# Kernel tuning notes

Hardware: AMD Instinct MI355X
Metric: run time of the kernel (lower is better)

## Reference

```python
import jax, jax.numpy as jnp
import numpy as np

WS = 8          # window size
NUM_HEADS = 3
DIM = 96
HIDDEN = int(DIM * 2.0)
LN_EPS = 1e-5


def _rel_pos_index(ws):
    coords = np.stack(np.meshgrid(np.arange(ws), np.arange(ws), indexing='ij'))  # (2,ws,ws)
    cf = coords.reshape(2, -1)                          # (2, N)
    rel = cf[:, :, None] - cf[:, None, :]               # (2, N, N)
    rel = rel.transpose(1, 2, 0).astype(np.int64)       # (N, N, 2)
    rel[:, :, 0] += ws - 1
    rel[:, :, 1] += ws - 1
    rel[:, :, 0] *= 2 * ws - 1
    return jnp.asarray(rel.sum(-1))                     # (N, N)


def _layernorm(x, g, b):
    mu = jnp.mean(x, axis=-1, keepdims=True)
    var = jnp.mean(jnp.square(x - mu), axis=-1, keepdims=True)
    return (x - mu) * jax.lax.rsqrt(var + LN_EPS) * g + b


def setup_inputs() -> dict:
    key = jax.random.key(0)
    ks = jax.random.split(key, 10)
    C = DIM
    std = 0.02
    return {
        'x': jax.random.normal(ks[0], (8, C, 256, 256), dtype=jnp.float32),
        'qkv_w': jax.random.normal(ks[1], (3 * C, C), dtype=jnp.float32) * std,
        'qkv_b': jnp.zeros((3 * C,), dtype=jnp.float32),
        'proj_w': jax.random.normal(ks[2], (C, C), dtype=jnp.float32) * std,
        'proj_b': jnp.zeros((C,), dtype=jnp.float32),
        'rpb_table': jax.random.normal(ks[3], ((2 * WS - 1) ** 2, NUM_HEADS), dtype=jnp.float32) * std,
        'norm1_g': jnp.ones((C,), dtype=jnp.float32),
        'norm1_b': jnp.zeros((C,), dtype=jnp.float32),
        'norm2_g': jnp.ones((C,), dtype=jnp.float32),
        'norm2_b': jnp.zeros((C,), dtype=jnp.float32),
        'fc1_w': jax.random.normal(ks[4], (HIDDEN, C), dtype=jnp.float32) * std,
        'fc1_b': jnp.zeros((HIDDEN,), dtype=jnp.float32),
        'fc2_w': jax.random.normal(ks[5], (C, HIDDEN), dtype=jnp.float32) * std,
        'fc2_b': jnp.zeros((C,), dtype=jnp.float32),
        'H': 256,
        'W': 256,
    }


def reference(x, qkv_w, qkv_b, proj_w, proj_b, rpb_table,
              norm1_g, norm1_b, norm2_g, norm2_b,
              fc1_w, fc1_b, fc2_w, fc2_b, H, W):
    B, C, Hc, Wc = x.shape
    ws = WS
    nh, nw = H // ws, W // ws
    N = ws * ws
    heads = NUM_HEADS
    hd = C // heads

    # window partition: (B,C,H,W) -> (B*nh*nw, N, C)
    xp = jnp.transpose(x, (0, 2, 3, 1))
    xw = xp.reshape(B, nh, ws, nw, ws, C).transpose(0, 1, 3, 2, 4, 5)
    xw = xw.reshape(B * nh * nw, N, C)

    xw = _layernorm(xw, norm1_g, norm1_b)

    # window attention
    B_ = B * nh * nw
    qkv = xw @ qkv_w.T + qkv_b                                  # (B_, N, 3C)
    qkv = qkv.reshape(B_, N, 3, heads, hd).transpose(2, 0, 3, 1, 4)
    q, k, v = qkv[0], qkv[1], qkv[2]                            # (B_, h, N, d)
    q = q * (hd ** -0.5)
    attn = jnp.einsum('bhnd,bhmd->bhnm', q, k)                  # (B_, h, N, N)
    rpi = _rel_pos_index(ws)                                    # (N, N)
    bias = rpb_table[rpi.reshape(-1)].reshape(N, N, heads).transpose(2, 0, 1)
    attn = jax.nn.softmax(attn + bias[None], axis=-1)
    out = jnp.einsum('bhnm,bhmd->bhnd', attn, v)                # (B_, h, N, d)
    out = out.transpose(0, 2, 1, 3).reshape(B_, N, C)
    out = out @ proj_w.T + proj_b

    # norm2 + MLP (note: original applies them sequentially, single residual at end)
    out = _layernorm(out, norm2_g, norm2_b)
    h = jax.nn.gelu(out @ fc1_w.T + fc1_b, approximate=False)
    out = h @ fc2_w.T + fc2_b

    # window merge + residual
    out = out.reshape(B, nh, nw, ws, ws, C).transpose(0, 5, 1, 3, 2, 4)
    out = out.reshape(B, C, H, W)
    return out + x
```

## Files before the change

kernel.cpp:

```cpp
#include <hip/hip_runtime.h>
#include <hip/hip_bf16.h>

using bf16 = __hip_bfloat16;
typedef short short8  __attribute__((ext_vector_type(8)));
typedef short short4v __attribute__((ext_vector_type(4)));
typedef float f32x4   __attribute__((ext_vector_type(4)));

static __device__ __forceinline__ bf16  f2b(float v){ return __float2bfloat16(v); }
static __device__ __forceinline__ float s2f(short s){ return __bfloat162float(__builtin_bit_cast(bf16, s)); }
static __device__ __forceinline__ short f2s(float f){ return __builtin_bit_cast(short, __float2bfloat16(f)); }

static __device__ __forceinline__ short8 ldw8(const float* __restrict__ p){
  const float4 u = *(const float4*)(p);
  const float4 v = *(const float4*)(p + 4);
  short8 r;
  r[0]=f2s(u.x); r[1]=f2s(u.y); r[2]=f2s(u.z); r[3]=f2s(u.w);
  r[4]=f2s(v.x); r[5]=f2s(v.y); r[6]=f2s(v.z); r[7]=f2s(v.w);
  return r;
}

#define MFMA16(a,b,c) __builtin_amdgcn_mfma_f32_16x16x32_bf16((a),(b),(c),0,0,0)

#define KEYR(row) ((((row) >> 2) & 3) << 4)

constexpr int TPB = 256;
constexpr float EPS = 1e-5f;
constexpr float QSC = 0.17677669529663687f;

constexpr int WQ_OFF  = 0;
constexpr int WPJ_OFF = 27648;
constexpr int WF1_OFF = 36864;
constexpr int WF2_OFF = 55296;
constexpr int WTOT    = 73728;
constexpr int BTAB_BYTE_OFF = 147456;
constexpr size_t WS_NEEDED = 147456 + 49152;

constexpr int R0_OFF = 0;
constexpr int R1_OFF = 26624;
constexpr int R2_OFF = 53248;
constexpr int SMEM_BYTES = 80896;

__global__ void init_ws_kernel(
    const float* __restrict__ qkvw, const float* __restrict__ projw,
    const float* __restrict__ fc1w, const float* __restrict__ fc2w,
    const float* __restrict__ rpb,
    bf16* __restrict__ wbf, float* __restrict__ btab)
{
  const int i = blockIdx.x * 256 + threadIdx.x;
  if (i < WTOT){
    float v;
    if (i < WPJ_OFF)      v = qkvw[i];
    else if (i < WF1_OFF) v = projw[i - WPJ_OFF];
    else if (i < WF2_OFF) v = fc1w[i - WF1_OFF];
    else                  v = fc2w[i - WF2_OFF];
    if (i < 9216) v *= QSC;
    wbf[i] = f2b(v);
  }
  if (i < 3*64*64){
    const int h   = i >> 12;
    const int row = (i >> 6) & 63;
    const int col = i & 63;
    const int rel = ((row>>3) - (col>>3) + 7)*15 + ((row&7) - (col&7) + 7);
    btab[i] = rpb[rel*3 + h];
  }
}

template<bool PRE>
__global__ __launch_bounds__(TPB, 2) void swin_block_kernel(
    const float* __restrict__ x,
    const float* __restrict__ qkvw,  const float* __restrict__ qkvb,
    const float* __restrict__ projw, const float* __restrict__ projb,
    const float* __restrict__ rpb,
    const float* __restrict__ n1g,   const float* __restrict__ n1b,
    const float* __restrict__ n2g,   const float* __restrict__ n2b,
    const float* __restrict__ fc1w,  const float* __restrict__ fc1b,
    const float* __restrict__ fc2w,  const float* __restrict__ fc2b,
    float* __restrict__ out,
    const bf16* __restrict__ wbf,    const float* __restrict__ btab)
{
  __shared__ alignas(16) unsigned char smem[SMEM_BYTES];
  char* s_a  = (char*)(smem + R0_OFF);
  char* s_q  = (char*)(smem + R0_OFF);
  char* s_k  = (char*)(smem + R0_OFF + 10240);
  char* s_at = (char*)(smem + R0_OFF);
  char* s_ao = (char*)(smem + R1_OFF);
  char* s_h  = (char*)(smem + R1_OFF);
  char* s_vt = (char*)(smem + R2_OFF);
  char* s_p  = (char*)(smem + R2_OFF + 9216);

  const bf16* wQ  = wbf + WQ_OFF;
  const bf16* wP  = wbf + WPJ_OFF;
  const bf16* wF1 = wbf + WF1_OFF;
  const bf16* wF2 = wbf + WF2_OFF;

  const int tid  = threadIdx.x;
  const int wid  = tid >> 6;
  const int lane = tid & 63;
  const int quad = lane >> 4;
  const int l15  = lane & 15;
  const int m0   = wid * 16;
  const int row0 = m0 + quad * 4;
  const int cwz  = quad << 4;
  const int rwz  = ((l15 >> 2) & 3) << 4;

  const int blk = blockIdx.x;
  const int b    = blk >> 9;
  const int wh   = (blk >> 4) & 31;
  const int wcol = blk & 15;
  const size_t base = ((size_t)b * 96) * 65536 + (size_t)wh * 2048 + (size_t)wcol * 16;

  float4 xsave[12];
  #pragma unroll
  for (int it = 0; it < 12; it++){
    const int idx4 = it*256 + tid;
    const int c = idx4 >> 5, r = idx4 & 31;
    const int irow = r >> 2, j0 = (r & 3) * 4;
    const float4 xv = *(const float4*)(x + base + (size_t)c*65536 + irow*256 + j0);
    xsave[it] = xv;
    const int srow = (j0 >> 3)*64 + irow*8 + (j0 & 7);
    const int co = (c*2) ^ KEYR(srow);
    *(bf16*)(s_a + (srow+0)*208 + co) = f2b(xv.x);
    *(bf16*)(s_a + (srow+1)*208 + co) = f2b(xv.y);
    *(bf16*)(s_a + (srow+2)*208 + co) = f2b(xv.z);
    *(bf16*)(s_a + (srow+3)*208 + co) = f2b(xv.w);
  }
  __syncthreads();

  {
    const int rr = tid >> 2, s = tid & 3;
    const int cb = s*24;
    const int key = KEYR(rr);
    float gv[24], bb[24];
    #pragma unroll
    for (int u = 0; u < 6; u++){
      const float4 g4 = *(const float4*)(n1g + cb + u*4);
      const float4 b4 = *(const float4*)(n1b + cb + u*4);
      gv[u*4+0]=g4.x; gv[u*4+1]=g4.y; gv[u*4+2]=g4.z; gv[u*4+3]=g4.w;
      bb[u*4+0]=b4.x; bb[u*4+1]=b4.y; bb[u*4+2]=b4.z; bb[u*4+3]=b4.w;
    }
    #pragma unroll
    for (int wv = 0; wv < 2; wv++){
      char* row = s_a + (wv*64 + rr)*208;
      float vals[24];
      float sum = 0.f, sq = 0.f;
      #pragma unroll
      for (int u = 0; u < 3; u++){
        short8 v8 = *(const short8*)(row + (((cb + u*8)*2) ^ key));
        #pragma unroll
        for (int j = 0; j < 8; j++){ float f = s2f(v8[j]); vals[u*8+j] = f; sum += f; sq += f*f; }
      }
      sum += __shfl_xor(sum, 1); sum += __shfl_xor(sum, 2);
      sq  += __shfl_xor(sq , 1); sq  += __shfl_xor(sq , 2);
      const float mu  = sum * (1.f/96.f);
      const float inv = rsqrtf(fmaxf(sq*(1.f/96.f) - mu*mu, 0.f) + EPS);
      #pragma unroll
      for (int u = 0; u < 3; u++){
        short8 o8;
        #pragma unroll
        for (int j = 0; j < 8; j++)
          o8[j] = f2s((vals[u*8+j] - mu) * inv * gv[u*8+j] + bb[u*8+j]);
        *(short8*)(row + (((cb + u*8)*2) ^ key)) = o8;
      }
    }
  }

  const f32x4 zac = {0.f, 0.f, 0.f, 0.f};

  short8 A0[2], A1[2], A2[2];
  #pragma unroll
  for (int wv = 0; wv < 2; wv++){
    const char* ap = s_a + (wv*64 + m0 + l15)*208;
    const int q16 = (quad*16) ^ rwz;
    A0[wv] = *(const short8*)(ap + q16);
    A1[wv] = *(const short8*)(ap + q16 + 64);
    A2[wv] = *(const short8*)(ap + q16 + 128);
  }
  __syncthreads();

  for (int h = 0; h < 3; h++){
    #pragma unroll
    for (int nt = 0; nt < 6; nt++){
      const int sect = nt >> 1;
      const int d = (nt & 1)*16 + l15;
      const int wrow = sect*96 + h*32 + d;
      short8 w0, w1, w2;
      if constexpr (PRE){
        const bf16* wp = wQ + wrow*96 + quad*8;
        w0 = *(const short8*)(wp);
        w1 = *(const short8*)(wp + 32);
        w2 = *(const short8*)(wp + 64);
      } else {
        const float* wp = qkvw + wrow*96 + quad*8;
        w0 = ldw8(wp); w1 = ldw8(wp + 32); w2 = ldw8(wp + 64);
      }
      float bias = qkvb[wrow];
      if (PRE && sect == 0) bias *= QSC;
      const f32x4 bacc = {bias, bias, bias, bias};
      #pragma unroll
      for (int wv = 0; wv < 2; wv++){
        f32x4 acc = bacc;
        acc = MFMA16(A0[wv], w0, acc);
        acc = MFMA16(A1[wv], w1, acc);
        acc = MFMA16(A2[wv], w2, acc);
        if (sect == 0){
          #pragma unroll
          for (int r = 0; r < 4; r++){
            const float qv = PRE ? acc[r] : acc[r]*QSC;
            *(bf16*)(s_q + (wv*64 + row0 + r)*80 + ((d*2) ^ cwz)) = f2b(qv);
          }
        } else if (sect == 1){
          #pragma unroll
          for (int r = 0; r < 4; r++)
            *(bf16*)(s_k + (wv*64 + row0 + r)*80 + ((d*2) ^ cwz)) = f2b(acc[r]);
        } else {
          short4v pk;
          #pragma unroll
          for (int r = 0; r < 4; r++) pk[r] = f2s(acc[r]);
          *(short4v*)(s_vt + wv*4608 + d*144 + ((row0*2) ^ KEYR(d))) = pk;
        }
      }
    }
    __syncthreads();

    {
      f32x4 bvv[4];
      if constexpr (PRE){
        #pragma unroll
        for (int nt = 0; nt < 4; nt++)
          #pragma unroll
          for (int r = 0; r < 4; r++)
            bvv[nt][r] = btab[(h*64 + row0 + r)*64 + nt*16 + l15];
      } else {
        #pragma unroll
        for (int nt = 0; nt < 4; nt++){
          const int col = nt*16 + l15, ci = col >> 3, cj = col & 7;
          #pragma unroll
          for (int r = 0; r < 4; r++){
            const int row = row0 + r, ri = row >> 3, rj = row & 7;
            const int rel = (ri - ci + 7)*15 + (rj - cj + 7);
            bvv[nt][r] = rpb[rel*3 + h];
          }
        }
      }
      #pragma unroll
      for (int wv = 0; wv < 2; wv++){
        const int q16 = (quad*16) ^ rwz;
        const short8 aq = *(const short8*)(s_q + (wv*64 + m0 + l15)*80 + q16);
        f32x4 sc[4];
        #pragma unroll
        for (int nt = 0; nt < 4; nt++){
          const short8 bk = *(const short8*)(s_k + (wv*64 + nt*16 + l15)*80 + q16);
          sc[nt] = MFMA16(aq, bk, bvv[nt]);
        }
        #pragma unroll
        for (int r = 0; r < 4; r++){
          const float e0 = __expf(fminf(sc[0][r], 80.f));
          const float e1 = __expf(fminf(sc[1][r], 80.f));
          const float e2 = __expf(fminf(sc[2][r], 80.f));
          const float e3 = __expf(fminf(sc[3][r], 80.f));
          float sm = e0+e1+e2+e3;
          sm += __shfl_xor(sm, 1);
          sm += __shfl_xor(sm, 2);
          sm += __shfl_xor(sm, 4);
          sm += __shfl_xor(sm, 8);
          const float rs = 1.f / sm;
          char* pb = s_p + (wv*64 + row0 + r)*144;
          *(bf16*)(pb + ((      l15*2) ^ cwz)) = f2b(e0*rs);
          *(bf16*)(pb + (( 32 + l15*2) ^ cwz)) = f2b(e1*rs);
          *(bf16*)(pb + (( 64 + l15*2) ^ cwz)) = f2b(e2*rs);
          *(bf16*)(pb + (( 96 + l15*2) ^ cwz)) = f2b(e3*rs);
        }

        const char* pr = s_p + (wv*64 + m0 + l15)*144;
        const short8 p0 = *(const short8*)(pr + q16);
        const short8 p1 = *(const short8*)(pr + q16 + 64);
        #pragma unroll
        for (int nt = 0; nt < 2; nt++){
          const char* vr = s_vt + wv*4608 + (nt*16 + l15)*144;
          f32x4 acc = zac;
          acc = MFMA16(p0, *(const short8*)(vr + q16), acc);
          acc = MFMA16(p1, *(const short8*)(vr + q16 + 64), acc);
          #pragma unroll
          for (int r = 0; r < 4; r++)
            *(bf16*)(s_ao + (wv*64 + row0 + r)*208 + (((h*32 + nt*16 + l15)*2) ^ cwz)) = f2b(acc[r]);
        }
      }
    }
    __syncthreads();
  }

  {
    short8 B0[2], B1[2], B2[2];
    #pragma unroll
    for (int wv = 0; wv < 2; wv++){
      const char* bp = s_ao + (wv*64 + m0 + l15)*208;
      const int q16 = (quad*16) ^ rwz;
      B0[wv] = *(const short8*)(bp + q16);
      B1[wv] = *(const short8*)(bp + q16 + 64);
      B2[wv] = *(const short8*)(bp + q16 + 128);
    }
    float g6[6], b6[6];
    #pragma unroll
    for (int nt = 0; nt < 6; nt++){
      g6[nt] = n2g[nt*16 + l15];
      b6[nt] = n2b[nt*16 + l15];
    }
    float vals[2][6][4];
    #pragma unroll
    for (int nt = 0; nt < 6; nt++){
      const int wrow = nt*16 + l15;
      short8 w0, w1, w2;
      if constexpr (PRE){
        const bf16* wp = wP + wrow*96 + quad*8;
        w0 = *(const short8*)(wp);
        w1 = *(const short8*)(wp + 32);
        w2 = *(const short8*)(wp + 64);
      } else {
        const float* wp = projw + wrow*96 + quad*8;
        w0 = ldw8(wp); w1 = ldw8(wp + 32); w2 = ldw8(wp + 64);
      }
      const float bias = projb[wrow];
      const f32x4 bacc = {bias, bias, bias, bias};
      #pragma unroll
      for (int wv = 0; wv < 2; wv++){
        f32x4 acc = bacc;
        acc = MFMA16(B0[wv], w0, acc);
        acc = MFMA16(B1[wv], w1, acc);
        acc = MFMA16(B2[wv], w2, acc);
        #pragma unroll
        for (int r = 0; r < 4; r++) vals[wv][nt][r] = acc[r];
      }
    }
    #pragma unroll
    for (int wv = 0; wv < 2; wv++){
      #pragma unroll
      for (int r = 0; r < 4; r++){
        float sm = 0.f, sq = 0.f;
        #pragma unroll
        for (int nt = 0; nt < 6; nt++){ const float v = vals[wv][nt][r]; sm += v; sq += v*v; }
        sm += __shfl_xor(sm, 1); sm += __shfl_xor(sm, 2);
        sm += __shfl_xor(sm, 4); sm += __shfl_xor(sm, 8);
        sq += __shfl_xor(sq, 1); sq += __shfl_xor(sq, 2);
        sq += __shfl_xor(sq, 4); sq += __shfl_xor(sq, 8);
        const float mu  = sm * (1.f/96.f);
        const float inv = rsqrtf(fmaxf(sq*(1.f/96.f) - mu*mu, 0.f) + EPS);
        char* ob = s_a + (wv*64 + row0 + r)*208;
        #pragma unroll
        for (int nt = 0; nt < 6; nt++)
          *(bf16*)(ob + (((nt*16 + l15)*2) ^ cwz)) =
              f2b((vals[wv][nt][r] - mu) * inv * g6[nt] + b6[nt]);
      }
    }
  }
  __syncthreads();

  {
    short8 C0[2], C1[2], C2[2];
    #pragma unroll
    for (int wv = 0; wv < 2; wv++){
      const char* cp = s_a + (wv*64 + m0 + l15)*208;
      const int q16 = (quad*16) ^ rwz;
      C0[wv] = *(const short8*)(cp + q16);
      C1[wv] = *(const short8*)(cp + q16 + 64);
      C2[wv] = *(const short8*)(cp + q16 + 128);
    }
    #pragma unroll
    for (int nt = 0; nt < 12; nt++){
      const int wrow = nt*16 + l15;
      short8 w0, w1, w2;
      if constexpr (PRE){
        const bf16* wp = wF1 + wrow*96 + quad*8;
        w0 = *(const short8*)(wp);
        w1 = *(const short8*)(wp + 32);
        w2 = *(const short8*)(wp + 64);
      } else {
        const float* wp = fc1w + wrow*96 + quad*8;
        w0 = ldw8(wp); w1 = ldw8(wp + 32); w2 = ldw8(wp + 64);
      }
      const float bias = fc1b[wrow];
      const f32x4 bacc = {bias, bias, bias, bias};
      #pragma unroll
      for (int wv = 0; wv < 2; wv++){
        f32x4 acc = bacc;
        acc = MFMA16(C0[wv], w0, acc);
        acc = MFMA16(C1[wv], w1, acc);
        acc = MFMA16(C2[wv], w2, acc);
        #pragma unroll
        for (int r = 0; r < 4; r++){
          const float v = acc[r];
          const float t = __expf(1.5957691216057308f * (v + 0.044715f*v*v*v));
          const float g = v - v * (1.f / (t + 1.f));
          *(bf16*)(s_h + (wv*64 + row0 + r)*400 + ((wrow*2) ^ cwz)) = f2b(g);
        }
      }
    }
  }
  __syncthreads();

  {
    short8 F[2][6];
    #pragma unroll
    for (int wv = 0; wv < 2; wv++){
      const char* fp = s_h + (wv*64 + m0 + l15)*400;
      const int q16 = (quad*16) ^ rwz;
      #pragma unroll
      for (int ks = 0; ks < 6; ks++)
        F[wv][ks] = *(const short8*)(fp + ks*64 + q16);
    }
    #pragma unroll
    for (int nt = 0; nt < 6; nt++){
      const int wrow = nt*16 + l15;
      short8 w[6];
      if constexpr (PRE){
        const bf16* wp = wF2 + wrow*192 + quad*8;
        #pragma unroll
        for (int ks = 0; ks < 6; ks++) w[ks] = *(const short8*)(wp + ks*32);
      } else {
        const float* wp = fc2w + wrow*192 + quad*8;
        #pragma unroll
        for (int ks = 0; ks < 6; ks++) w[ks] = ldw8(wp + ks*32);
      }
      const float bias = fc2b[wrow];
      const f32x4 bacc = {bias, bias, bias, bias};
      #pragma unroll
      for (int wv = 0; wv < 2; wv++){
        f32x4 acc = bacc;
        #pragma unroll
        for (int ks = 0; ks < 6; ks++)
          acc = MFMA16(F[wv][ks], w[ks], acc);
        short4v pk;
        #pragma unroll
        for (int r = 0; r < 4; r++) pk[r] = f2s(acc[r]);
        *(short4v*)(s_at + wrow*272 + (wv*64 + row0)*2) = pk;
      }
    }
  }
  __syncthreads();

  #pragma unroll
  for (int it = 0; it < 12; it++){
    const int idx4 = it*256 + tid;
    const int c = idx4 >> 5, r = idx4 & 31;
    const int irow = r >> 2, j0 = (r & 3) * 4;
    const int t0 = (j0 >> 3)*64 + irow*8 + (j0 & 7);
    const short4v pv = *(const short4v*)(s_at + c*272 + t0*2);
    const size_t g = base + (size_t)c*65536 + irow*256 + j0;
    const float4 xv = xsave[it];
    float4 ov;
    ov.x = xv.x + s2f(pv[0]);
    ov.y = xv.y + s2f(pv[1]);
    ov.z = xv.z + s2f(pv[2]);
    ov.w = xv.w + s2f(pv[3]);
    *(float4*)(out + g) = ov;
  }
}

extern "C" void kernel_launch(void* const* d_in, const int* in_sizes, int n_in,
                              void* d_out, int out_size, void* d_ws, size_t ws_size,
                              hipStream_t stream) {
  const float* x     = (const float*)d_in[0];
  const float* qkvw  = (const float*)d_in[1];
  const float* qkvb  = (const float*)d_in[2];
  const float* projw = (const float*)d_in[3];
  const float* projb = (const float*)d_in[4];
  const float* rpb   = (const float*)d_in[5];
  const float* n1g   = (const float*)d_in[6];
  const float* n1b   = (const float*)d_in[7];
  const float* n2g   = (const float*)d_in[8];
  const float* n2b   = (const float*)d_in[9];
  const float* fc1w  = (const float*)d_in[10];
  const float* fc1b  = (const float*)d_in[11];
  const float* fc2w  = (const float*)d_in[12];
  const float* fc2b  = (const float*)d_in[13];
  float* out = (float*)d_out;

  if (ws_size >= WS_NEEDED && d_ws != nullptr) {
    bf16*  wbf  = (bf16*)d_ws;
    float* btab = (float*)((char*)d_ws + BTAB_BYTE_OFF);
    init_ws_kernel<<<dim3(288), dim3(256), 0, stream>>>(
        qkvw, projw, fc1w, fc2w, rpb, wbf, btab);
    swin_block_kernel<true><<<dim3(4096), dim3(TPB), 0, stream>>>(
        x, qkvw, qkvb, projw, projb, rpb,
        n1g, n1b, n2g, n2b, fc1w, fc1b, fc2w, fc2b, out, wbf, btab);
  } else {
    swin_block_kernel<false><<<dim3(4096), dim3(TPB), 0, stream>>>(
        x, qkvw, qkvb, projw, projb, rpb,
        n1g, n1b, n2g, n2b, fc1w, fc1b, fc2w, fc2b, out,
        (const bf16*)nullptr, (const float*)nullptr);
  }
}
```

Measured before the change: 618.2 us.

## Shrink LDS footprint, register-resident softmax, split MLP hidden dim for 3 blocks/CU

New measurement: 670.3 us. 1.08x slower.

```diff
diff --git a/kernel.cpp b/kernel.cpp
--- a/kernel.cpp
+++ b/kernel.cpp
@@ -5,10 +5,15 @@
 typedef short short8  __attribute__((ext_vector_type(8)));
 typedef short short4v __attribute__((ext_vector_type(4)));
 typedef float f32x4   __attribute__((ext_vector_type(4)));
+typedef unsigned int  uint;
+typedef uint uint4v   __attribute__((ext_vector_type(4)));
 
 static __device__ __forceinline__ bf16  f2b(float v){ return __float2bfloat16(v); }
 static __device__ __forceinline__ float s2f(short s){ return __bfloat162float(__builtin_bit_cast(bf16, s)); }
 static __device__ __forceinline__ short f2s(float f){ return __builtin_bit_cast(short, __float2bfloat16(f)); }
+static __device__ __forceinline__ uint pk2(float lo, float hi){
+  return (uint)(unsigned short)f2s(lo) | ((uint)(unsigned short)f2s(hi) << 16);
+}
 
 static __device__ __forceinline__ short8 ldw8(const float* __restrict__ p){
   const float4 u = *(const float4*)(p);
@@ -21,8 +26,6 @@
 
 #define MFMA16(a,b,c) __builtin_amdgcn_mfma_f32_16x16x32_bf16((a),(b),(c),0,0,0)
 
-#define KEYR(row) ((((row) >> 2) & 3) << 4)
-
 constexpr int TPB = 256;
 constexpr float EPS = 1e-5f;
 constexpr float QSC = 0.17677669529663687f;
@@ -35,10 +38,9 @@
 constexpr int BTAB_BYTE_OFF = 147456;
 constexpr size_t WS_NEEDED = 147456 + 49152;
 
-constexpr int R0_OFF = 0;
-constexpr int R1_OFF = 26624;
-constexpr int R2_OFF = 53248;
-constexpr int SMEM_BYTES = 80896;
+constexpr int A_OFF = 0;
+constexpr int B_OFF = 24576;
+constexpr int SMEM_BYTES = 49152;
 
 __global__ void init_ws_kernel(
     const float* __restrict__ qkvw, const float* __restrict__ projw,
@@ -66,7 +68,7 @@
 }
 
 template<bool PRE>
-__global__ __launch_bounds__(TPB, 2) void swin_block_kernel(
+__global__ __launch_bounds__(TPB, 3) void swin_block_kernel(
     const float* __restrict__ x,
     const float* __restrict__ qkvw,  const float* __restrict__ qkvb,
     const float* __restrict__ projw, const float* __restrict__ projb,
@@ -79,14 +81,13 @@
     const bf16* __restrict__ wbf,    const float* __restrict__ btab)
 {
   __shared__ alignas(16) unsigned char smem[SMEM_BYTES];
-  char* s_a  = (char*)(smem + R0_OFF);
-  char* s_q  = (char*)(smem + R0_OFF);
-  char* s_k  = (char*)(smem + R0_OFF + 10240);
-  char* s_at = (char*)(smem + R0_OFF);
-  char* s_ao = (char*)(smem + R1_OFF);
-  char* s_h  = (char*)(smem + R1_OFF);
-  char* s_vt = (char*)(smem + R2_OFF);
-  char* s_p  = (char*)(smem + R2_OFF + 9216);
+  char* s_a  = (char*)(smem + A_OFF);
+  char* s_q  = (char*)(smem + A_OFF);
+  char* s_k  = (char*)(smem + A_OFF + 8192);
+  char* s_vt = (char*)(smem + A_OFF + 16384);
+  char* s_at = (char*)(smem + A_OFF);
+  char* s_ao = (char*)(smem + B_OFF);
+  char* s_h  = (char*)(smem + B_OFF);
 
   const bf16* wQ  = wbf + WQ_OFF;
   const bf16* wP  = wbf + WPJ_OFF;
@@ -94,14 +95,12 @@
   const bf16* wF2 = wbf + WF2_OFF;
 
   const int tid  = threadIdx.x;
+  const int lane = tid & 63;
   const int wid  = tid >> 6;
-  const int lane = tid & 63;
   const int quad = lane >> 4;
   const int l15  = lane & 15;
   const int m0   = wid * 16;
   const int row0 = m0 + quad * 4;
-  const int cwz  = quad << 4;
-  const int rwz  = ((l15 >> 2) & 3) << 4;
 
   const int blk = blockIdx.x;
   const int b    = blk >> 9;
@@ -109,27 +108,23 @@
   const int wcol = blk & 15;
   const size_t base = ((size_t)b * 96) * 65536 + (size_t)wh * 2048 + (size_t)wcol * 16;
 
-  float4 xsave[12];
   #pragma unroll
   for (int it = 0; it < 12; it++){
     const int idx4 = it*256 + tid;
     const int c = idx4 >> 5, r = idx4 & 31;
     const int irow = r >> 2, j0 = (r & 3) * 4;
     const float4 xv = *(const float4*)(x + base + (size_t)c*65536 + irow*256 + j0);
-    xsave[it] = xv;
     const int srow = (j0 >> 3)*64 + irow*8 + (j0 & 7);
-    const int co = (c*2) ^ KEYR(srow);
-    *(bf16*)(s_a + (srow+0)*208 + co) = f2b(xv.x);
-    *(bf16*)(s_a + (srow+1)*208 + co) = f2b(xv.y);
-    *(bf16*)(s_a + (srow+2)*208 + co) = f2b(xv.z);
-    *(bf16*)(s_a + (srow+3)*208 + co) = f2b(xv.w);
+    *(bf16*)(s_a + (srow+0)*192 + c*2) = f2b(xv.x);
+    *(bf16*)(s_a + (srow+1)*192 + c*2) = f2b(xv.y);
+    *(bf16*)(s_a + (srow+2)*192 + c*2) = f2b(xv.z);
+    *(bf16*)(s_a + (srow+3)*192 + c*2) = f2b(xv.w);
   }
   __syncthreads();
 
   {
     const int rr = tid >> 2, s = tid & 3;
     const int cb = s*24;
-    const int key = KEYR(rr);
     float gv[24], bb[24];
     #pragma unroll
     for (int u = 0; u < 6; u++){
@@ -140,12 +135,12 @@
     }
     #pragma unroll
     for (int wv = 0; wv < 2; wv++){
-      char* row = s_a + (wv*64 + rr)*208;
+      char* row = s_a + (wv*64 + rr)*192 + cb*2;
       float vals[24];
       float sum = 0.f, sq = 0.f;
       #pragma unroll
       for (int u = 0; u < 3; u++){
-        short8 v8 = *(const short8*)(row + (((cb + u*8)*2) ^ key));
+        short8 v8 = *(const short8*)(row + u*16);
         #pragma unroll
         for (int j = 0; j < 8; j++){ float f = s2f(v8[j]); vals[u*8+j] = f; sum += f; sq += f*f; }
       }
@@ -159,7 +154,7 @@
         #pragma unroll
         for (int j = 0; j < 8; j++)
           o8[j] = f2s((vals[u*8+j] - mu) * inv * gv[u*8+j] + bb[u*8+j]);
-        *(short8*)(row + (((cb + u*8)*2) ^ key)) = o8;
+        *(short8*)(row + u*16) = o8;
       }
     }
   }
@@ -169,11 +164,10 @@
   short8 A0[2], A1[2], A2[2];
   #pragma unroll
   for (int wv = 0; wv < 2; wv++){
-    const char* ap = s_a + (wv*64 + m0 + l15)*208;
-    const int q16 = (quad*16) ^ rwz;
-    A0[wv] = *(const short8*)(ap + q16);
-    A1[wv] = *(const short8*)(ap + q16 + 64);
-    A2[wv] = *(const short8*)(ap + q16 + 128);
+    const char* ap = s_a + (wv*64 + m0 + l15)*192 + quad*16;
+    A0[wv] = *(const short8*)(ap);
+    A1[wv] = *(const short8*)(ap + 64);
+    A2[wv] = *(const short8*)(ap + 128);
   }
   __syncthreads();
 
@@ -206,84 +200,91 @@
           #pragma unroll
           for (int r = 0; r < 4; r++){
             const float qv = PRE ? acc[r] : acc[r]*QSC;
-            *(bf16*)(s_q + (wv*64 + row0 + r)*80 + ((d*2) ^ cwz)) = f2b(qv);
+            *(bf16*)(s_q + (wv*64 + row0 + r)*64 + d*2) = f2b(qv);
           }
         } else if (sect == 1){
           #pragma unroll
           for (int r = 0; r < 4; r++)
-            *(bf16*)(s_k + (wv*64 + row0 + r)*80 + ((d*2) ^ cwz)) = f2b(acc[r]);
+            *(bf16*)(s_k + (wv*64 + row0 + r)*64 + d*2) = f2b(acc[r]);
         } else {
-          short4v pk;
+          short4v pkv;
           #pragma unroll
-          for (int r = 0; r < 4; r++) pk[r] = f2s(acc[r]);
-          *(short4v*)(s_vt + wv*4608 + d*144 + ((row0*2) ^ KEYR(d))) = pk;
+          for (int r = 0; r < 4; r++) pkv[r] = f2s(acc[r]);
+          *(short4v*)(s_vt + wv*4096 + d*128 + row0*2) = pkv;
         }
       }
     }
     __syncthreads();
 
-    {
-      f32x4 bvv[4];
-      if constexpr (PRE){
-        #pragma unroll
-        for (int nt = 0; nt < 4; nt++)
-          #pragma unroll
-          for (int r = 0; r < 4; r++)
-            bvv[nt][r] = btab[(h*64 + row0 + r)*64 + nt*16 + l15];
-      } else {
-        #pragma unroll
-        for (int nt = 0; nt < 4; nt++){
-          const int col = nt*16 + l15, ci = col >> 3, cj = col & 7;
+    #pragma unroll
+    for (int wv = 0; wv < 2; wv++){
+      const short8 bq = *(const short8*)(s_q + (wv*64 + m0 + l15)*64 + quad*16);
+      f32x4 st[4];
+      #pragma unroll
+      for (int nt = 0; nt < 4; nt++){
+        f32x4 bb;
+        if constexpr (PRE){
+          const float4 b4 = *(const float4*)(btab + (h*64 + m0 + l15)*64 + nt*16 + quad*4);
+          bb[0]=b4.x; bb[1]=b4.y; bb[2]=b4.z; bb[3]=b4.w;
+        } else {
+          const int q = m0 + l15, qi = q >> 3, qj = q & 7;
           #pragma unroll
           for (int r = 0; r < 4; r++){
-            const int row = row0 + r, ri = row >> 3, rj = row & 7;
-            const int rel = (ri - ci + 7)*15 + (rj - cj + 7);
-            bvv[nt][r] = rpb[rel*3 + h];
+            const int k = nt*16 + quad*4 + r, ki = k >> 3, kj = k & 7;
+            bb[r] = rpb[((qi - ki + 7)*15 + (qj - kj + 7))*3 + h];
           }
         }
-      }
-      #pragma unroll
-      for (int wv = 0; wv < 2; wv++){
-        const int q16 = (quad*16) ^ rwz;
-        const short8 aq = *(const short8*)(s_q + (wv*64 + m0 + l15)*80 + q16);
-        f32x4 sc[4];
-        #pragma unroll
-        for (int nt = 0; nt < 4; nt++){
-          const short8 bk = *(const short8*)(s_k + (wv*64 + nt*16 + l15)*80 + q16);
-          sc[nt] = MFMA16(aq, bk, bvv[nt]);
-        }
+        const short8 ak = *(const short8*)(s_k + (wv*64 + nt*16 + l15)*64 + quad*16);
+        st[nt] = MFMA16(ak, bq, bb);
+      }
+      float e[16];
+      float tot = 0.f;
+      #pragma unroll
+      for (int nt = 0; nt < 4; nt++)
         #pragma unroll
         for (int r = 0; r < 4; r++){
-          const float e0 = __expf(fminf(sc[0][r], 80.f));
-          const float e1 = __expf(fminf(sc[1][r], 80.f));
-          const float e2 = __expf(fminf(sc[2][r], 80.f));
-          const float e3 = __expf(fminf(sc[3][r], 80.f));
-          float sm = e0+e1+e2+e3;
-          sm += __shfl_xor(sm, 1);
-          sm += __shfl_xor(sm, 2);
-          sm += __shfl_xor(sm, 4);
-          sm += __shfl_xor(sm, 8);
-          const float rs = 1.f / sm;
-          char* pb = s_p + (wv*64 + row0 + r)*144;
-          *(bf16*)(pb + ((      l15*2) ^ cwz)) = f2b(e0*rs);
-          *(bf16*)(pb + (( 32 + l15*2) ^ cwz)) = f2b(e1*rs);
-          *(bf16*)(pb + (( 64 + l15*2) ^ cwz)) = f2b(e2*rs);
-          *(bf16*)(pb + (( 96 + l15*2) ^ cwz)) = f2b(e3*rs);
-        }
-
-        const char* pr = s_p + (wv*64 + m0 + l15)*144;
-        const short8 p0 = *(const short8*)(pr + q16);
-        const short8 p1 = *(const short8*)(pr + q16 + 64);
-        #pragma unroll
-        for (int nt = 0; nt < 2; nt++){
-          const char* vr = s_vt + wv*4608 + (nt*16 + l15)*144;
-          f32x4 acc = zac;
-          acc = MFMA16(p0, *(const short8*)(vr + q16), acc);
-          acc = MFMA16(p1, *(const short8*)(vr + q16 + 64), acc);
-          #pragma unroll
-          for (int r = 0; r < 4; r++)
-            *(bf16*)(s_ao + (wv*64 + row0 + r)*208 + (((h*32 + nt*16 + l15)*2) ^ cwz)) = f2b(acc[r]);
-        }
+          const float v = __expf(fminf(st[nt][r], 80.f));
+          e[nt*4+r] = v; tot += v;
+        }
+      tot += __shfl_xor(tot, 16);
+      tot += __shfl_xor(tot, 32);
+      const float rs = 1.f / tot;
+      uint pk[8];
+      #pragma unroll
+      for (int nt = 0; nt < 4; nt++){
+        pk[nt*2+0] = pk2(e[nt*4+0]*rs, e[nt*4+1]*rs);
+        pk[nt*2+1] = pk2(e[nt*4+2]*rs, e[nt*4+3]*rs);
+      }
+      const int lane0 = (quad & 1)*32 + l15;
+      const int lane1 = lane0 + 16;
+      const bool hiq = quad >= 2;
+      short8 pa[2];
+      #pragma unroll
+      for (int s = 0; s < 2; s++){
+        const uint aA0 = __shfl(pk[4*s+0], lane0);
+        const uint aA1 = __shfl(pk[4*s+1], lane0);
+        const uint aB0 = __shfl(pk[4*s+2], lane0);
+        const uint aB1 = __shfl(pk[4*s+3], lane0);
+        const uint cA0 = __shfl(pk[4*s+0], lane1);
+        const uint cA1 = __shfl(pk[4*s+1], lane1);
+        const uint cB0 = __shfl(pk[4*s+2], lane1);
+        const uint cB1 = __shfl(pk[4*s+3], lane1);
+        uint4v u;
+        u[0] = hiq ? aB0 : aA0;
+        u[1] = hiq ? aB1 : aA1;
+        u[2] = hiq ? cB0 : cA0;
+        u[3] = hiq ? cB1 : cA1;
+        pa[s] = __builtin_bit_cast(short8, u);
+      }
+      #pragma unroll
+      for (int ntv = 0; ntv < 2; ntv++){
+        const char* vr = s_vt + wv*4096 + (ntv*16 + l15)*128 + quad*16;
+        f32x4 acc = zac;
+        acc = MFMA16(pa[0], *(const short8*)(vr), acc);
+        acc = MFMA16(pa[1], *(const short8*)(vr + 64), acc);
+        #pragma unroll
+        for (int r = 0; r < 4; r++)
+          *(bf16*)(s_ao + (wv*64 + row0 + r)*192 + (h*32 + ntv*16 + l15)*2) = f2b(acc[r]);
       }
     }
     __syncthreads();
@@ -293,11 +294,10 @@
     short8 B0[2], B1[2], B2[2];
     #pragma unroll
     for (int wv = 0; wv < 2; wv++){
-      const char* bp = s_ao + (wv*64 + m0 + l15)*208;
-      const int q16 = (quad*16) ^ rwz;
-      B0[wv] = *(const short8*)(bp + q16);
-      B1[wv] = *(const short8*)(bp + q16 + 64);
-      B2[wv] = *(const short8*)(bp + q16 + 128);
+      const char* bp = s_ao + (wv*64 + m0 + l15)*192 + quad*16;
+      B0[wv] = *(const short8*)(bp);
+      B1[wv] = *(const short8*)(bp + 64);
+      B2[wv] = *(const short8*)(bp + 128);
     }
     float g6[6], b6[6];
     #pragma unroll
@@ -344,94 +344,108 @@
         sq += __shfl_xor(sq, 4); sq += __shfl_xor(sq, 8);
         const float mu  = sm * (1.f/96.f);
         const float inv = rsqrtf(fmaxf(sq*(1.f/96.f) - mu*mu, 0.f) + EPS);
-        char* ob = s_a + (wv*64 + row0 + r)*208;
+        char* ob = s_a + (wv*64 + row0 + r)*192;
         #pragma unroll
         for (int nt = 0; nt < 6; nt++)
-          *(bf16*)(ob + (((nt*16 + l15)*2) ^ cwz)) =
+          *(bf16*)(ob + (nt*16 + l15)*2) =
               f2b((vals[wv][nt][r] - mu) * inv * g6[nt] + b6[nt]);
       }
     }
   }
-  __syncthreads();
 
   {
     short8 C0[2], C1[2], C2[2];
     #pragma unroll
     for (int wv = 0; wv < 2; wv++){
-      const char* cp = s_a + (wv*64 + m0 + l15)*208;
-      const int q16 = (quad*16) ^ rwz;
-      C0[wv] = *(const short8*)(cp + q16);
-      C1[wv] = *(const short8*)(cp + q16 + 64);
-      C2[wv] = *(const short8*)(cp + q16 + 128);
-    }
-    #pragma unroll
-    for (int nt = 0; nt < 12; nt++){
-      const int wrow = nt*16 + l15;
-      short8 w0, w1, w2;
-      if constexpr (PRE){
-        const bf16* wp = wF1 + wrow*96 + quad*8;
-        w0 = *(const short8*)(wp);
-        w1 = *(const short8*)(wp + 32);
-        w2 = *(const short8*)(wp + 64);
-      } else {
-        const float* wp = fc1w + wrow*96 + quad*8;
-        w0 = ldw8(wp); w1 = ldw8(wp + 32); w2 = ldw8(wp + 64);
-      }
-      const float bias = fc1b[wrow];
-      const f32x4 bacc = {bias, bias, bias, bias};
+      const char* cp = s_a + (wv*64 + m0 + l15)*192 + quad*16;
+      C0[wv] = *(const short8*)(cp);
+      C1[wv] = *(const short8*)(cp + 64);
+      C2[wv] = *(const short8*)(cp + 128);
+    }
+    __syncthreads();
+
+    f32x4 acc2[2][6];
+    #pragma unroll
+    for (int nt = 0; nt < 6; nt++){
+      const float bias = fc2b[nt*16 + l15];
       #pragma unroll
       for (int wv = 0; wv < 2; wv++){
-        f32x4 acc = bacc;
-        acc = MFMA16(C0[wv], w0, acc);
-        acc = MFMA16(C1[wv], w1, acc);
-        acc = MFMA16(C2[wv], w2, acc);
-        #pragma unroll
-        for (int r = 0; r < 4; r++){
-          const float v = acc[r];
-          const float t = __expf(1.5957691216057308f * (v + 0.044715f*v*v*v));
-          const float g = v - v * (1.f / (t + 1.f));
-          *(bf16*)(s_h + (wv*64 + row0 + r)*400 + ((wrow*2) ^ cwz)) = f2b(g);
-        }
-      }
-    }
-  }
-  __syncthreads();
-
-  {
-    short8 F[2][6];
-    #pragma unroll
-    for (int wv = 0; wv < 2; wv++){
-      const char* fp = s_h + (wv*64 + m0 + l15)*400;
-      const int q16 = (quad*16) ^ rwz;
-      #pragma unroll
-      for (int ks = 0; ks < 6; ks++)
-        F[wv][ks] = *(const short8*)(fp + ks*64 + q16);
-    }
+        acc2[wv][nt][0] = bias; acc2[wv][nt][1] = bias;
+        acc2[wv][nt][2] = bias; acc2[wv][nt][3] = bias;
+      }
+    }
+
+    #pragma unroll
+    for (int half = 0; half < 2; half++){
+      #pragma unroll
+      for (int nt = 0; nt < 6; nt++){
+        const int wrow = half*96 + nt*16 + l15;
+        short8 w0, w1, w2;
+        if constexpr (PRE){
+          const bf16* wp = wF1 + wrow*96 + quad*8;
+          w0 = *(const short8*)(wp);
+          w1 = *(const short8*)(wp + 32);
+          w2 = *(const short8*)(wp + 64);
+        } else {
+          const float* wp = fc1w + wrow*96 + quad*8;
+          w0 = ldw8(wp); w1 = ldw8(wp + 32); w2 = ldw8(wp + 64);
+        }
+        const float bias = fc1b[wrow];
+        const f32x4 bacc = {bias, bias, bias, bias};
+        #pragma unroll
+        for (int wv = 0; wv < 2; wv++){
+          f32x4 acc = bacc;
+          acc = MFMA16(C0[wv], w0, acc);
+          acc = MFMA16(C1[wv], w1, acc);
+          acc = MFMA16(C2[wv], w2, acc);
+          #pragma unroll
+          for (int r = 0; r < 4; r++){
+            const float v = acc[r];
+            const float t = __expf(1.5957691216057308f * (v + 0.044715f*v*v*v));
+            const float g = v - v * (1.f / (t + 1.f));
+            *(bf16*)(s_h + (wv*64 + row0 + r)*192 + (nt*16 + l15)*2) = f2b(g);
+          }
+        }
+      }
+      short8 F0[2], F1[2], F2[2];
+      #pragma unroll
+      for (int wv = 0; wv < 2; wv++){
+        const char* fp = s_h + (wv*64 + m0 + l15)*192 + quad*16;
+        F0[wv] = *(const short8*)(fp);
+        F1[wv] = *(const short8*)(fp + 64);
+        F2[wv] = *(const short8*)(fp + 128);
+      }
+      #pragma unroll
+      for (int nt = 0; nt < 6; nt++){
+        const int wrow = nt*16 + l15;
+        short8 w0, w1, w2;
+        if constexpr (PRE){
+          const bf16* wp = wF2 + wrow*192 + half*96 + quad*8;
+          w0 = *(const short8*)(wp);
+          w1 = *(const short8*)(wp + 32);
+          w2 = *(const short8*)(wp + 64);
+        } else {
+          const float* wp = fc2w + wrow*192 + half*96 + quad*8;
+          w0 = ldw8(wp); w1 = ldw8(wp + 32); w2 = ldw8(wp + 64);
+        }
+        #pragma unroll
+        for (int wv = 0; wv < 2; wv++){
+          acc2[wv][nt] = MFMA16(F0[wv], w0, acc2[wv][nt]);
+          acc2[wv][nt] = MFMA16(F1[wv], w1, acc2[wv][nt]);
+          acc2[wv][nt] = MFMA16(F2[wv], w2, acc2[wv][nt]);
+        }
+      }
+    }
+
     #pragma unroll
     for (int nt = 0; nt < 6; nt++){
       const int wrow = nt*16 + l15;
-      short8 w[6];
-      if constexpr (PRE){
-        const bf16* wp = wF2 + wrow*192 + quad*8;
-        #pragma unroll
-        for (int ks = 0; ks < 6; ks++) w[ks] = *(const short8*)(wp + ks*32);
-      } else {
-        const float* wp = fc2w + wrow*192 + quad*8;
-        #pragma unroll
-        for (int ks = 0; ks < 6; ks++) w[ks] = ldw8(wp + ks*32);
-      }
-      const float bias = fc2b[wrow];
-      const f32x4 bacc = {bias, bias, bias, bias};
       #pragma unroll
       for (int wv = 0; wv < 2; wv++){
-        f32x4 acc = bacc;
-        #pragma unroll
-        for (int ks = 0; ks < 6; ks++)
-          acc = MFMA16(F[wv][ks], w[ks], acc);
-        short4v pk;
-        #pragma unroll
-        for (int r = 0; r < 4; r++) pk[r] = f2s(acc[r]);
-        *(short4v*)(s_at + wrow*272 + (wv*64 + row0)*2) = pk;
+        short4v pkv;
+        #pragma unroll
+        for (int r = 0; r < 4; r++) pkv[r] = f2s(acc2[wv][nt][r]);
+        *(short4v*)(s_at + wrow*256 + (wv*64 + row0)*2) = pkv;
       }
     }
   }
@@ -443,9 +457,9 @@
     const int c = idx4 >> 5, r = idx4 & 31;
     const int irow = r >> 2, j0 = (r & 3) * 4;
     const int t0 = (j0 >> 3)*64 + irow*8 + (j0 & 7);
-    const short4v pv = *(const short4v*)(s_at + c*272 + t0*2);
+    const short4v pv = *(const short4v*)(s_at + c*256 + t0*2);
     const size_t g = base + (size_t)c*65536 + irow*256 + j0;
-    const float4 xv = xsave[it];
+    const float4 xv = *(const float4*)(x + g);
     float4 ov;
     ov.x = xv.x + s2f(pv[0]);
     ov.y = xv.y + s2f(pv[1]);
```
